# Kernel tuning notes

Hardware: AMD Instinct MI355X
Metric: run time of the kernel (lower is better)

The kernel has to match this reference:

```python
import jax, jax.numpy as jnp
import numpy as np

B, C_IN, C_OUT, H, W = 4, 64, 64, 64, 64
D = 2 * C_OUT  # projected channel dim = 128


def conv1x1(x, w, b):
    # x: [B,Cin,H,W], w: [Cout,Cin], b: [Cout]
    return jnp.einsum('bchw,oc->bohw', x, w) + b[None, :, None, None]


def setup_inputs() -> dict:
    key = jax.random.key(0)
    ks = jax.random.split(key, 10)
    s_q = 1.0 / np.sqrt(C_IN)
    s_kv = 1.0 / np.sqrt(2 * C_IN)
    s_o = 1.0 / np.sqrt(D)
    return {
        'x_upper': jax.random.normal(ks[0], (B, C_IN, H, W), jnp.float32),
        'x_lower': jax.random.normal(ks[1], (B, 2 * C_IN, H, W), jnp.float32),
        'wq': jax.random.uniform(ks[2], (D, C_IN), jnp.float32, -s_q, s_q),
        'bq': jax.random.uniform(ks[3], (D,), jnp.float32, -s_q, s_q),
        'wk': jax.random.uniform(ks[4], (D, 2 * C_IN), jnp.float32, -s_kv, s_kv),
        'bk': jax.random.uniform(ks[5], (D,), jnp.float32, -s_kv, s_kv),
        'wv': jax.random.uniform(ks[6], (D, 2 * C_IN), jnp.float32, -s_kv, s_kv),
        'bv': jax.random.uniform(ks[7], (D,), jnp.float32, -s_kv, s_kv),
        'wo': jax.random.uniform(ks[8], (D, D), jnp.float32, -s_o, s_o),
        'bo': jax.random.uniform(ks[9], (D,), jnp.float32, -s_o, s_o),
    }


def reference(x_upper, x_lower, wq, bq, wk, bk, wv, bv, wo, bo):
    q = conv1x1(x_upper, wq, bq)   # [B,D,H,W]
    k = conv1x1(x_lower, wk, bk)   # [B,D,H,W]
    v = conv1x1(x_lower, wv, bv)   # [B,D,H,W]
    b, d = q.shape[0], q.shape[1]
    # NOTE: the torch code uses .view (raw reshape), NOT a transpose --
    # faithful translation is a plain reshape of the contiguous NCHW tensor.
    qf = q.reshape(b, -1, d)       # [B, N, D], N = H*W
    kf = k.reshape(b, -1, d)
    vf = v.reshape(b, -1, d)
    scores = jnp.einsum('bnd,bmd->bnm', qf, kf) / (d ** 0.5)  # [B,N,N]
    attn = jax.nn.softmax(scores, axis=-1)
    of = jnp.einsum('bnm,bmd->bnd', attn, vf)  # [B,N,D]
    out = of.reshape(v.shape)                  # [B,D,H,W]
    out = conv1x1(out, wo, bo) + x_lower
    return out
```

## Files before the change

kernel.cpp:

```cpp
#include <hip/hip_runtime.h>
#include <math.h>

#define BB 4
#define CIN 64
#define CL 128
#define DD 128
#define HW 4096
#define NN 4096
#define TP 132

typedef __attribute__((ext_vector_type(8))) __bf16 bf16x8;
typedef __attribute__((ext_vector_type(16))) float f32x16;

__device__ __forceinline__ unsigned short f2bf(float f) {
    unsigned u = __builtin_bit_cast(unsigned, f);
    u += 0x7fffu + ((u >> 16) & 1u);
    return (unsigned short)(u >> 16);
}
__device__ __forceinline__ unsigned pack2(float lo, float hi) {
    return (unsigned)f2bf(lo) | ((unsigned)f2bf(hi) << 16);
}
__device__ __forceinline__ float bf2f(unsigned s) {
    return __builtin_bit_cast(float, s << 16);
}
__device__ __forceinline__ unsigned pack_trunc(float lo, float hi) {
    return __builtin_amdgcn_perm(__builtin_bit_cast(unsigned, hi),
                                 __builtin_bit_cast(unsigned, lo), 0x07060302u);
}
__device__ __forceinline__ float exp2_fast(float x) {
#if __has_builtin(__builtin_amdgcn_exp2f)
    return __builtin_amdgcn_exp2f(x);
#else
    return __expf(x * 0.6931471805599453f);
#endif
}
__device__ __forceinline__ void async_copy16(const unsigned short* g,
                                             unsigned short* l) {
    __builtin_amdgcn_global_load_lds(
        (const __attribute__((address_space(1))) void*)g,
        (__attribute__((address_space(3))) void*)l, 16, 0, 0);
}

__global__ __launch_bounds__(256) void proj_q_kernel(
    const float* __restrict__ x, const float* __restrict__ w,
    const float* __restrict__ bias, unsigned short* __restrict__ out,
    float oscale)
{
    int blk = blockIdx.x;
    int chunk = blk & 15;
    int og = (blk >> 4) & 15;
    int b = blk >> 8;
    int o0 = og * 8;
    int px = chunk * 256 + threadIdx.x;

    float acc[8];
#pragma unroll
    for (int oo = 0; oo < 8; ++oo) acc[oo] = bias[o0 + oo];
    const float* xb = x + (size_t)b * CIN * HW + px;
#pragma unroll 4
    for (int c = 0; c < CIN; ++c) {
        float xv = xb[(size_t)c * HW];
#pragma unroll
        for (int oo = 0; oo < 8; ++oo)
            acc[oo] += xv * w[(o0 + oo) * CIN + c];
    }
#pragma unroll
    for (int oo = 0; oo < 8; ++oo) {
        size_t oidx = ((size_t)b * 128 + o0 + oo) * HW + px;
        out[oidx] = f2bf(acc[oo] * oscale);
    }
}

__global__ __launch_bounds__(256) void proj_kv_kernel(
    const float* __restrict__ x,
    const float* __restrict__ wk, const float* __restrict__ bk,
    const float* __restrict__ wv, const float* __restrict__ bv,
    unsigned short* __restrict__ kout, unsigned short* __restrict__ vout)
{
    int blk = blockIdx.x;
    int chunk = blk & 15;
    int og = (blk >> 4) & 15;
    int b = blk >> 8;
    int o0 = og * 8;
    int px = chunk * 256 + threadIdx.x;

    float ack[8], acv[8];
#pragma unroll
    for (int oo = 0; oo < 8; ++oo) {
        ack[oo] = bk[o0 + oo];
        acv[oo] = bv[o0 + oo];
    }
    const float* xb = x + (size_t)b * CL * HW + px;
#pragma unroll 4
    for (int c = 0; c < CL; ++c) {
        float xv = xb[(size_t)c * HW];
#pragma unroll
        for (int oo = 0; oo < 8; ++oo) {
            ack[oo] += xv * wk[(o0 + oo) * CL + c];
            acv[oo] += xv * wv[(o0 + oo) * CL + c];
        }
    }
    int nlo = px >> 7;
    int xs = (((px >> 3) & 15) ^ (nlo & 15)) * 8 + (px & 7);
    unsigned short* kb = kout + (size_t)b * NN * DD + (size_t)nlo * 128 + xs;
#pragma unroll
    for (int oo = 0; oo < 8; ++oo) {
        kb[(size_t)(o0 + oo) * 4096] = f2bf(ack[oo]);
        size_t oidx = ((size_t)b * 128 + o0 + oo) * HW + px;
        vout[oidx] = f2bf(acv[oo]);
    }
}

__global__ __launch_bounds__(256) void proj_o_kernel(
    const unsigned short* __restrict__ x, const float* __restrict__ w,
    const float* __restrict__ bias, const float* __restrict__ resid,
    float* __restrict__ out)
{
    int blk = blockIdx.x;
    int chunk = blk & 15;
    int og = (blk >> 4) & 15;
    int b = blk >> 8;
    int o0 = og * 8;
    int px = chunk * 256 + threadIdx.x;

    float acc[8];
#pragma unroll
    for (int oo = 0; oo < 8; ++oo) acc[oo] = bias[o0 + oo];
    const unsigned short* xb = x + (size_t)b * DD * HW + px;
#pragma unroll 4
    for (int c = 0; c < DD; ++c) {
        float xv = bf2f((unsigned)xb[(size_t)c * HW]);
#pragma unroll
        for (int oo = 0; oo < 8; ++oo)
            acc[oo] += xv * w[(o0 + oo) * DD + c];
    }
#pragma unroll
    for (int oo = 0; oo < 8; ++oo) {
        size_t oidx = ((size_t)b * 128 + o0 + oo) * HW + px;
        out[oidx] = acc[oo] + resid[oidx];
    }
}

__global__ __launch_bounds__(256) void transpose_v(
    const unsigned short* __restrict__ vf, unsigned short* __restrict__ vt)
{
    __shared__ unsigned short tld[64 * TP];
    int tid = threadIdx.x;
    int b = blockIdx.x >> 6;
    int n0 = (blockIdx.x & 63) * 64;
    const unsigned short* src = vf + (size_t)b * NN * DD + (size_t)n0 * DD;
#pragma unroll
    for (int i = 0; i < 4; ++i) {
        int ch = tid + i * 256;
        int n = ch >> 4, x = ch & 15;
        union { uint4 q; unsigned long long u[2]; } t;
        t.q = *(const uint4*)(src + (size_t)n * DD + x * 8);
        unsigned short* d = &tld[n * TP + x * 8];
        *(unsigned long long*)(d) = t.u[0];
        *(unsigned long long*)(d + 4) = t.u[1];
    }
    __syncthreads();
    unsigned short* dst = vt + (size_t)b * NN * DD + (size_t)(n0 >> 7) * 16384;
    int xb_ = (n0 & 127) >> 3;
#pragma unroll
    for (int i = 0; i < 4; ++i) {
        int ch = tid + i * 256;
        int g = ch & 7, d = ch >> 3;
        union { uint4 q; unsigned short s[8]; } t;
#pragma unroll
        for (int j = 0; j < 8; ++j) t.s[j] = tld[(g * 8 + j) * TP + d];
        int xs = (xb_ + g) ^ (d & 15);
        *(uint4*)(dst + (size_t)d * 128 + xs * 8) = t.q;
    }
}

__global__ __launch_bounds__(512) void attn_mfma(
    const unsigned short* __restrict__ qf, const unsigned short* __restrict__ kfs,
    const unsigned short* __restrict__ vts, unsigned short* __restrict__ of)
{
    __shared__ __align__(16) char smem[133632];

    const int tid = threadIdx.x;
    const int lane = tid & 63;
    const int w = tid >> 6;
    const int kq = w & 3;
    const int rh = w >> 2;
    const int half = lane >> 5;
    const int l5 = lane & 31;
    const int b = blockIdx.x >> 6;
    const int rb0 = (blockIdx.x & 63) * 64;
    const int rw0 = rb0 + rh * 32;
    const int cw = kq * 32;

    const unsigned short* qb = qf + (size_t)b * NN * DD;
    const unsigned short* kb = kfs + (size_t)b * NN * DD;
    const unsigned short* vb = vts + (size_t)b * NN * DD;

    bf16x8 qfrag[8];
    {
        const unsigned short* qrow = qb + (size_t)(rw0 + l5) * DD + half * 8;
#pragma unroll
        for (int kk = 0; kk < 8; ++kk)
            qfrag[kk] = *(const bf16x8*)(qrow + kk * 16);
    }

    f32x16 O[4] = {};
    float lacc = 0.f;

    auto stage = [&](int t, int buf) {
        const unsigned short* kt = kb + (size_t)t * 16384;
        const unsigned short* vt_ = vb + (size_t)t * 16384;
        unsigned short* kl = (unsigned short*)(smem + buf * 65536);
        unsigned short* vl = kl + 16384;
#pragma unroll
        for (int j = 0; j < 4; ++j) {
            int c = (w * 4 + j) * 512;
            async_copy16(kt + c + lane * 8, kl + c);
            async_copy16(vt_ + c + lane * 8, vl + c);
        }
    };

    stage(0, 0);
    stage(1, 1);

    const int NT = NN / 128;
    for (int t = 0; t < NT; ++t) {
        const int cur = t & 1;
        if (t < NT - 1) asm volatile("s_waitcnt vmcnt(8)" ::: "memory");
        else            asm volatile("s_waitcnt vmcnt(0)" ::: "memory");
        __builtin_amdgcn_s_barrier();
        asm volatile("" ::: "memory");

        const unsigned short* kl = (const unsigned short*)(smem + cur * 65536);
        const unsigned short* vl = kl + 16384;

        f32x16 S = {};
#pragma unroll
        for (int kk = 0; kk < 8; ++kk) {
            bf16x8 kfr = *(const bf16x8*)
                &kl[(cw + l5) * 128 + (((kk * 2 + half) ^ (l5 & 15)) * 8)];
            S = __builtin_amdgcn_mfma_f32_32x32x16_bf16(kfr, qfrag[kk], S, 0, 0, 0);
        }

        float p[16];
#pragma unroll
        for (int r = 0; r < 16; ++r) p[r] = exp2_fast(S[r]);
        {
            float t0 = (p[0] + p[1]) + (p[2] + p[3]);
            float t1 = (p[4] + p[5]) + (p[6] + p[7]);
            float t2 = (p[8] + p[9]) + (p[10] + p[11]);
            float t3 = (p[12] + p[13]) + (p[14] + p[15]);
            lacc += (t0 + t1) + (t2 + t3);
        }

#pragma unroll
        for (int kc = 0; kc < 2; ++kc) {
            unsigned PA0 = pack_trunc(p[8 * kc + 0], p[8 * kc + 1]);
            unsigned PA1 = pack_trunc(p[8 * kc + 2], p[8 * kc + 3]);
            unsigned PB0 = pack_trunc(p[8 * kc + 4], p[8 * kc + 5]);
            unsigned PB1 = pack_trunc(p[8 * kc + 6], p[8 * kc + 7]);
            unsigned snd0 = half ? PA0 : PB0;
            unsigned snd1 = half ? PA1 : PB1;
            unsigned rcv0 = (unsigned)__shfl_xor((int)snd0, 32, 64);
            unsigned rcv1 = (unsigned)__shfl_xor((int)snd1, 32, 64);
            union { unsigned u[4]; bf16x8 v; } pf;
            pf.u[0] = half ? rcv0 : PA0;
            pf.u[1] = half ? rcv1 : PA1;
            pf.u[2] = half ? PB0 : rcv0;
            pf.u[3] = half ? PB1 : rcv1;
#pragma unroll
            for (int ds = 0; ds < 4; ++ds) {
                bf16x8 vfr = *(const bf16x8*)
                    &vl[(ds * 32 + l5) * 128 +
                        (((kq * 4 + kc * 2 + half) ^ (l5 & 15)) * 8)];
                O[ds] = __builtin_amdgcn_mfma_f32_32x32x16_bf16(vfr, pf.v, O[ds], 0, 0, 0);
            }
        }

        asm volatile("s_waitcnt lgkmcnt(0)" ::: "memory");
        __builtin_amdgcn_s_barrier();
        asm volatile("" ::: "memory");
        if (t + 2 < NT) stage(t + 2, cur);
    }

    lacc += __shfl_xor(lacc, 32, 64);

    float (*red_o)[64][129] = (float (*)[64][129])smem;
    float* red_l = (float*)(smem + 132096);
    if (half == 0) red_l[kq * 64 + rh * 32 + l5] = lacc;
#pragma unroll
    for (int ds = 0; ds < 4; ++ds)
#pragma unroll
        for (int r = 0; r < 16; ++r) {
            int d = ds * 32 + (r & 3) + 8 * (r >> 2) + 4 * half;
            red_o[kq][rh * 32 + l5][d] = O[ds][r];
        }
    __syncthreads();

    {
        int q = tid >> 3;
        int dg = tid & 7;
        float l = red_l[q] + red_l[64 + q] + red_l[128 + q] + red_l[192 + q];
        float inv = 1.f / l;
        unsigned outw[8];
#pragma unroll
        for (int i = 0; i < 8; ++i) {
            int d0 = dg * 16 + i * 2;
            float s0 = red_o[0][q][d0] + red_o[1][q][d0] +
                       red_o[2][q][d0] + red_o[3][q][d0];
            float s1 = red_o[0][q][d0 + 1] + red_o[1][q][d0 + 1] +
                       red_o[2][q][d0 + 1] + red_o[3][q][d0 + 1];
            outw[i] = pack2(s0 * inv, s1 * inv);
        }
        unsigned short* ob = of + (size_t)b * NN * DD + (size_t)(rb0 + q) * DD + dg * 16;
        *(uint4*)(ob) = *(uint4*)&outw[0];
        *(uint4*)(ob + 8) = *(uint4*)&outw[4];
    }
}

extern "C" void kernel_launch(void* const* d_in, const int* in_sizes, int n_in,
                              void* d_out, int out_size, void* d_ws, size_t ws_size,
                              hipStream_t stream) {
    const float* x_upper = (const float*)d_in[0];
    const float* x_lower = (const float*)d_in[1];
    const float* wq = (const float*)d_in[2];
    const float* bq = (const float*)d_in[3];
    const float* wk = (const float*)d_in[4];
    const float* bk = (const float*)d_in[5];
    const float* wv = (const float*)d_in[6];
    const float* bv = (const float*)d_in[7];
    const float* wo = (const float*)d_in[8];
    const float* bo = (const float*)d_in[9];
    float* out = (float*)d_out;

    const size_t ELT = (size_t)BB * NN * DD;
    unsigned short* qf  = (unsigned short*)d_ws;
    unsigned short* kfs = qf + ELT;
    unsigned short* vts = kfs + ELT;
    unsigned short* vfn = vts + ELT;
    unsigned short* ofb = vfn + ELT;

    const float qscale = (float)(0.08838834764831845 * 1.4426950408889634);

    proj_q_kernel<<<1024, 256, 0, stream>>>(x_upper, wq, bq, qf, qscale);
    proj_kv_kernel<<<1024, 256, 0, stream>>>(x_lower, wk, bk, wv, bv, kfs, vfn);
    transpose_v<<<256, 256, 0, stream>>>(vfn, vts);
    attn_mfma<<<BB * 64, 512, 0, stream>>>(qf, kfs, vts, ofb);
    proj_o_kernel<<<1024, 256, 0, stream>>>(ofb, wo, bo, x_lower, out);
}
```

Measured before the change: 181.5 us.

## Move 1x1 conv projections to bf16x3 split MFMA kernels and fuse Q/KV launches

Replaces the scalar-FMA Q, K/V and output projection kernels with MFMA-based kernels. They stage input tiles into LDS through async global-to-LDS copies and emulate fp32 precision with hi/lo bf16 splits: three products for QKV and two for the output projection, whose input is already bf16. The Q and KV projections are merged into one launch that dispatches on block index, and results are staged through LDS so they can be written as vectorized 16-byte stores in the swizzled K layout. This cuts the FMA-bound projection cost and one launch, at the cost of large LDS use (about 132KB) and fewer blocks, which limits occupancy.

```diff
diff --git a/kernel.cpp b/kernel.cpp
--- a/kernel.cpp
+++ b/kernel.cpp
@@ -8,6 +8,7 @@
 #define HW 4096
 #define NN 4096
 #define TP 132
+#define YP 136
 
 typedef __attribute__((ext_vector_type(8))) __bf16 bf16x8;
 typedef __attribute__((ext_vector_type(16))) float f32x16;
@@ -41,103 +42,296 @@
         (__attribute__((address_space(3))) void*)l, 16, 0, 0);
 }
 
-__global__ __launch_bounds__(256) void proj_q_kernel(
-    const float* __restrict__ x, const float* __restrict__ w,
-    const float* __restrict__ bias, unsigned short* __restrict__ out,
+__device__ __forceinline__ void split8(const float xv[8], bf16x8* hi, bf16x8* lo) {
+    union { unsigned u[4]; bf16x8 v; } H, L;
+#pragma unroll
+    for (int i = 0; i < 4; ++i) {
+        float x0 = xv[2 * i], x1 = xv[2 * i + 1];
+        H.u[i] = pack_trunc(x0, x1);
+        float h0 = __builtin_bit_cast(float,
+                     __builtin_bit_cast(unsigned, x0) & 0xffff0000u);
+        float h1 = __builtin_bit_cast(float,
+                     __builtin_bit_cast(unsigned, x1) & 0xffff0000u);
+        L.u[i] = pack_trunc(x0 - h0, x1 - h1);
+    }
+    *hi = H.v; *lo = L.v;
+}
+
+
+__global__ __launch_bounds__(512) void proj_qkv_mfma(
+    const float* __restrict__ xq, const float* __restrict__ wq,
+    const float* __restrict__ bq, unsigned short* __restrict__ qout,
+    const float* __restrict__ xl,
+    const float* __restrict__ wk, const float* __restrict__ bk,
+    const float* __restrict__ wv, const float* __restrict__ bv,
+    unsigned short* __restrict__ kout, unsigned short* __restrict__ vout,
     float oscale)
 {
-    int blk = blockIdx.x;
-    int chunk = blk & 15;
-    int og = (blk >> 4) & 15;
-    int b = blk >> 8;
-    int o0 = og * 8;
-    int px = chunk * 256 + threadIdx.x;
-
-    float acc[8];
-#pragma unroll
-    for (int oo = 0; oo < 8; ++oo) acc[oo] = bias[o0 + oo];
-    const float* xb = x + (size_t)b * CIN * HW + px;
-#pragma unroll 4
-    for (int c = 0; c < CIN; ++c) {
-        float xv = xb[(size_t)c * HW];
-#pragma unroll
-        for (int oo = 0; oo < 8; ++oo)
-            acc[oo] += xv * w[(o0 + oo) * CIN + c];
-    }
-#pragma unroll
-    for (int oo = 0; oo < 8; ++oo) {
-        size_t oidx = ((size_t)b * 128 + o0 + oo) * HW + px;
-        out[oidx] = f2bf(acc[oo] * oscale);
-    }
-}
-
-__global__ __launch_bounds__(256) void proj_kv_kernel(
-    const float* __restrict__ x,
-    const float* __restrict__ wk, const float* __restrict__ bk,
-    const float* __restrict__ wv, const float* __restrict__ bv,
-    unsigned short* __restrict__ kout, unsigned short* __restrict__ vout)
-{
-    int blk = blockIdx.x;
-    int chunk = blk & 15;
-    int og = (blk >> 4) & 15;
-    int b = blk >> 8;
-    int o0 = og * 8;
-    int px = chunk * 256 + threadIdx.x;
-
-    float ack[8], acv[8];
-#pragma unroll
-    for (int oo = 0; oo < 8; ++oo) {
-        ack[oo] = bk[o0 + oo];
-        acv[oo] = bv[o0 + oo];
-    }
-    const float* xb = x + (size_t)b * CL * HW + px;
-#pragma unroll 4
-    for (int c = 0; c < CL; ++c) {
-        float xv = xb[(size_t)c * HW];
-#pragma unroll
-        for (int oo = 0; oo < 8; ++oo) {
-            ack[oo] += xv * wk[(o0 + oo) * CL + c];
-            acv[oo] += xv * wv[(o0 + oo) * CL + c];
-        }
-    }
-    int nlo = px >> 7;
-    int xs = (((px >> 3) & 15) ^ (nlo & 15)) * 8 + (px & 7);
-    unsigned short* kb = kout + (size_t)b * NN * DD + (size_t)nlo * 128 + xs;
-#pragma unroll
-    for (int oo = 0; oo < 8; ++oo) {
-        kb[(size_t)(o0 + oo) * 4096] = f2bf(ack[oo]);
-        size_t oidx = ((size_t)b * 128 + o0 + oo) * HW + px;
-        vout[oidx] = f2bf(acv[oo]);
-    }
-}
-
-__global__ __launch_bounds__(256) void proj_o_kernel(
+    __shared__ __align__(16) char smem[135168];
+    float* xsf = (float*)smem;
+    unsigned short* ytk = (unsigned short*)(smem + 65536);
+    unsigned short* ytv = (unsigned short*)(smem + 100352);
+
+    const int tid = threadIdx.x;
+    const int w = tid >> 6;
+    const int lane = tid & 63;
+    const int half = lane >> 5;
+    const int l5 = lane & 31;
+
+    if (blockIdx.x < 128) {
+        const int b = blockIdx.x >> 5;
+        const int tile = blockIdx.x & 31;
+        const int px0 = tile * 128;
+        const int g = w >> 2;
+        const int ms = w & 3;
+
+        {
+            const float* src = xl + (size_t)b * CL * HW + px0
+                             + (size_t)(lane >> 5) * HW + (lane & 31) * 4;
+#pragma unroll
+            for (int k = 0; k < 8; ++k) {
+                int c = w * 8 + k;
+                async_copy16((const unsigned short*)(src + (size_t)(2 * c) * HW),
+                             (unsigned short*)(smem + c * 1024));
+            }
+        }
+
+        const float* wsrc = g ? wv : wk;
+        const float* bsrc = g ? bv : bk;
+        bf16x8 Ah[8], Al[8];
+        {
+            const float* wr = wsrc + (size_t)(ms * 32 + l5) * CL + half * 8;
+#pragma unroll
+            for (int ks = 0; ks < 8; ++ks) {
+                float tmp[8];
+                *(float4*)&tmp[0] = *(const float4*)(wr + ks * 16);
+                *(float4*)&tmp[4] = *(const float4*)(wr + ks * 16 + 4);
+                split8(tmp, &Ah[ks], &Al[ks]);
+            }
+        }
+        float biasr[16];
+#pragma unroll
+        for (int r = 0; r < 16; ++r)
+            biasr[r] = bsrc[ms * 32 + (r & 3) + 8 * (r >> 2) + 4 * half];
+
+        f32x16 acc[4];
+#pragma unroll
+        for (int ns = 0; ns < 4; ++ns)
+#pragma unroll
+            for (int r = 0; r < 16; ++r) acc[ns][r] = biasr[r];
+
+        asm volatile("s_waitcnt vmcnt(0)" ::: "memory");
+        __builtin_amdgcn_s_barrier();
+        asm volatile("" ::: "memory");
+
+#pragma unroll
+        for (int ns = 0; ns < 4; ++ns) {
+            int pxl = ns * 32 + l5;
+#pragma unroll
+            for (int ks = 0; ks < 8; ++ks) {
+                int kb_ = ks * 16 + half * 8;
+                float xv[8];
+#pragma unroll
+                for (int j = 0; j < 8; ++j)
+                    xv[j] = xsf[(kb_ + j) * 128 + pxl];
+                bf16x8 Bh, Bl;
+                split8(xv, &Bh, &Bl);
+                acc[ns] = __builtin_amdgcn_mfma_f32_32x32x16_bf16(Ah[ks], Bh, acc[ns], 0, 0, 0);
+                acc[ns] = __builtin_amdgcn_mfma_f32_32x32x16_bf16(Ah[ks], Bl, acc[ns], 0, 0, 0);
+                acc[ns] = __builtin_amdgcn_mfma_f32_32x32x16_bf16(Al[ks], Bh, acc[ns], 0, 0, 0);
+            }
+        }
+
+        unsigned short* yt = g ? ytv : ytk;
+#pragma unroll
+        for (int ns = 0; ns < 4; ++ns) {
+            int pxl = ns * 32 + l5;
+#pragma unroll
+            for (int r = 0; r < 16; ++r) {
+                int o = ms * 32 + (r & 3) + 8 * (r >> 2) + 4 * half;
+                yt[o * YP + pxl] = f2bf(acc[ns][r]);
+            }
+        }
+        __syncthreads();
+
+        unsigned short* kbase = kout + (size_t)b * NN * DD;
+        unsigned short* vbase = vout + (size_t)b * 128 * HW + px0;
+        const int tm = tile & 15;
+#pragma unroll
+        for (int i = 0; i < 4; ++i) {
+            int e = tid + i * 512;
+            int o = e >> 4, q = e & 15;
+            uint4 kq4 = *(const uint4*)(ytk + o * YP + q * 8);
+            *(uint4*)(kbase + (size_t)(o * 32 + tile) * 128 + ((q ^ tm) * 8)) = kq4;
+            uint4 vq4 = *(const uint4*)(ytv + o * YP + q * 8);
+            *(uint4*)(vbase + (size_t)o * HW + q * 8) = vq4;
+        }
+    } else {
+        const int qb_ = blockIdx.x - 128;
+        const int b = qb_ >> 5;
+        const int tile = qb_ & 31;
+        const int px0 = tile * 128;
+        const int ms = w & 3;
+        const int nsg = w >> 2;
+
+        {
+            const float* src = xq + (size_t)b * CIN * HW + px0
+                             + (size_t)(lane >> 5) * HW + (lane & 31) * 4;
+#pragma unroll
+            for (int k = 0; k < 4; ++k) {
+                int c = w * 4 + k;
+                async_copy16((const unsigned short*)(src + (size_t)(2 * c) * HW),
+                             (unsigned short*)(smem + c * 1024));
+            }
+        }
+
+        bf16x8 Ah[4], Al[4];
+        {
+            const float* wr = wq + (size_t)(ms * 32 + l5) * CIN + half * 8;
+#pragma unroll
+            for (int ks = 0; ks < 4; ++ks) {
+                float tmp[8];
+                *(float4*)&tmp[0] = *(const float4*)(wr + ks * 16);
+                *(float4*)&tmp[4] = *(const float4*)(wr + ks * 16 + 4);
+                split8(tmp, &Ah[ks], &Al[ks]);
+            }
+        }
+        float biasr[16];
+#pragma unroll
+        for (int r = 0; r < 16; ++r)
+            biasr[r] = bq[ms * 32 + (r & 3) + 8 * (r >> 2) + 4 * half];
+
+        f32x16 acc[2];
+#pragma unroll
+        for (int i = 0; i < 2; ++i)
+#pragma unroll
+            for (int r = 0; r < 16; ++r) acc[i][r] = biasr[r];
+
+        asm volatile("s_waitcnt vmcnt(0)" ::: "memory");
+        __builtin_amdgcn_s_barrier();
+        asm volatile("" ::: "memory");
+
+#pragma unroll
+        for (int i = 0; i < 2; ++i) {
+            int pxl = (nsg * 2 + i) * 32 + l5;
+#pragma unroll
+            for (int ks = 0; ks < 4; ++ks) {
+                int kb_ = ks * 16 + half * 8;
+                float xv[8];
+#pragma unroll
+                for (int j = 0; j < 8; ++j)
+                    xv[j] = xsf[(kb_ + j) * 128 + pxl];
+                bf16x8 Bh, Bl;
+                split8(xv, &Bh, &Bl);
+                acc[i] = __builtin_amdgcn_mfma_f32_32x32x16_bf16(Ah[ks], Bh, acc[i], 0, 0, 0);
+                acc[i] = __builtin_amdgcn_mfma_f32_32x32x16_bf16(Ah[ks], Bl, acc[i], 0, 0, 0);
+                acc[i] = __builtin_amdgcn_mfma_f32_32x32x16_bf16(Al[ks], Bh, acc[i], 0, 0, 0);
+            }
+        }
+
+#pragma unroll
+        for (int i = 0; i < 2; ++i) {
+            int pxl = (nsg * 2 + i) * 32 + l5;
+#pragma unroll
+            for (int r = 0; r < 16; ++r) {
+                int o = ms * 32 + (r & 3) + 8 * (r >> 2) + 4 * half;
+                ytk[o * YP + pxl] = f2bf(acc[i][r] * oscale);
+            }
+        }
+        __syncthreads();
+
+        unsigned short* qbase = qout + (size_t)b * 128 * HW + px0;
+#pragma unroll
+        for (int i = 0; i < 4; ++i) {
+            int e = tid + i * 512;
+            int o = e >> 4, q = e & 15;
+            uint4 qq4 = *(const uint4*)(ytk + o * YP + q * 8);
+            *(uint4*)(qbase + (size_t)o * HW + q * 8) = qq4;
+        }
+    }
+}
+
+__global__ __launch_bounds__(512) void proj_o_mfma(
     const unsigned short* __restrict__ x, const float* __restrict__ w,
     const float* __restrict__ bias, const float* __restrict__ resid,
     float* __restrict__ out)
 {
-    int blk = blockIdx.x;
-    int chunk = blk & 15;
-    int og = (blk >> 4) & 15;
-    int b = blk >> 8;
-    int o0 = og * 8;
-    int px = chunk * 256 + threadIdx.x;
-
-    float acc[8];
-#pragma unroll
-    for (int oo = 0; oo < 8; ++oo) acc[oo] = bias[o0 + oo];
-    const unsigned short* xb = x + (size_t)b * DD * HW + px;
-#pragma unroll 4
-    for (int c = 0; c < DD; ++c) {
-        float xv = bf2f((unsigned)xb[(size_t)c * HW]);
-#pragma unroll
-        for (int oo = 0; oo < 8; ++oo)
-            acc[oo] += xv * w[(o0 + oo) * DD + c];
-    }
-#pragma unroll
-    for (int oo = 0; oo < 8; ++oo) {
-        size_t oidx = ((size_t)b * 128 + o0 + oo) * HW + px;
-        out[oidx] = acc[oo] + resid[oidx];
+    __shared__ __align__(16) unsigned short xs16[128 * 128];
+
+    const int tid = threadIdx.x;
+    const int w_ = tid >> 6;
+    const int lane = tid & 63;
+    const int half = lane >> 5;
+    const int l5 = lane & 31;
+    const int b = blockIdx.x >> 5;
+    const int tile = blockIdx.x & 31;
+    const int px0 = tile * 128;
+    const int ms = w_ & 3;
+    const int nsg = w_ >> 2;
+
+    {
+        const unsigned short* src = x + (size_t)b * DD * HW + px0
+                                  + (size_t)(lane >> 4) * HW + (lane & 15) * 8;
+#pragma unroll
+        for (int k = 0; k < 4; ++k) {
+            int c = w_ * 4 + k;
+            async_copy16(src + (size_t)(4 * c) * HW, xs16 + c * 512);
+        }
+    }
+
+    bf16x8 Ah[8], Al[8];
+    {
+        const float* wr = w + (size_t)(ms * 32 + l5) * DD + half * 8;
+#pragma unroll
+        for (int ks = 0; ks < 8; ++ks) {
+            float tmp[8];
+            *(float4*)&tmp[0] = *(const float4*)(wr + ks * 16);
+            *(float4*)&tmp[4] = *(const float4*)(wr + ks * 16 + 4);
+            split8(tmp, &Ah[ks], &Al[ks]);
+        }
+    }
+    float biasr[16];
+#pragma unroll
+    for (int r = 0; r < 16; ++r)
+        biasr[r] = bias[ms * 32 + (r & 3) + 8 * (r >> 2) + 4 * half];
+
+    f32x16 acc[2];
+#pragma unroll
+    for (int i = 0; i < 2; ++i)
+#pragma unroll
+        for (int r = 0; r < 16; ++r) acc[i][r] = biasr[r];
+
+    asm volatile("s_waitcnt vmcnt(0)" ::: "memory");
+    __builtin_amdgcn_s_barrier();
+    asm volatile("" ::: "memory");
+
+#pragma unroll
+    for (int i = 0; i < 2; ++i) {
+        int pxl = (nsg * 2 + i) * 32 + l5;
+#pragma unroll
+        for (int ks = 0; ks < 8; ++ks) {
+            int kb_ = ks * 16 + half * 8;
+            union { unsigned u[4]; bf16x8 v; } B;
+#pragma unroll
+            for (int p = 0; p < 4; ++p) {
+                unsigned e0 = xs16[(kb_ + 2 * p) * 128 + pxl];
+                unsigned e1 = xs16[(kb_ + 2 * p + 1) * 128 + pxl];
+                B.u[p] = e0 | (e1 << 16);
+            }
+            acc[i] = __builtin_amdgcn_mfma_f32_32x32x16_bf16(Ah[ks], B.v, acc[i], 0, 0, 0);
+            acc[i] = __builtin_amdgcn_mfma_f32_32x32x16_bf16(Al[ks], B.v, acc[i], 0, 0, 0);
+        }
+    }
+
+#pragma unroll
+    for (int i = 0; i < 2; ++i) {
+        int px = px0 + (nsg * 2 + i) * 32 + l5;
+#pragma unroll
+        for (int r = 0; r < 16; ++r) {
+            int o = ms * 32 + (r & 3) + 8 * (r >> 2) + 4 * half;
+            size_t a = ((size_t)b * 128 + o) * HW + px;
+            out[a] = acc[i][r] + resid[a];
+        }
     }
 }
 
@@ -342,9 +536,10 @@
 
     const float qscale = (float)(0.08838834764831845 * 1.4426950408889634);
 
-    proj_q_kernel<<<1024, 256, 0, stream>>>(x_upper, wq, bq, qf, qscale);
-    proj_kv_kernel<<<1024, 256, 0, stream>>>(x_lower, wk, bk, wv, bv, kfs, vfn);
+    proj_qkv_mfma<<<256, 512, 0, stream>>>(x_upper, wq, bq, qf,
+                                           x_lower, wk, bk, wv, bv,
+                                           kfs, vfn, qscale);
     transpose_v<<<256, 256, 0, stream>>>(vfn, vts);
     attn_mfma<<<BB * 64, 512, 0, stream>>>(qf, kfs, vts, ofb);
-    proj_o_kernel<<<1024, 256, 0, stream>>>(ofb, wo, bo, x_lower, out);
-}
+    proj_o_mfma<<<128, 512, 0, stream>>>(ofb, wo, bo, x_lower, out);
+}
```

After: 153.9 us. 1.18x faster.
